# Kernel tuning notes

Hardware: AMD Instinct MI355X
Metric: run time of the kernel (lower is better)

Reference implementation:

```python
import jax, jax.numpy as jnp
import numpy as np


def setup_inputs() -> dict:
    key = jax.random.key(0)
    k1, k2 = jax.random.split(key)
    N, H, W, F = 32, 16, 16, 256
    B, C = 64, 8
    x = jax.random.normal(k1, (N, H, W, F), dtype=jnp.float32)
    # keras 'uniform' initializer: U(-0.05, 0.05)
    T = jax.random.uniform(k2, (F, B, C), dtype=jnp.float32, minval=-0.05, maxval=0.05)
    return {"x": x, "T": T}


def reference(x, T):
    # x: [N,H,W,F], T: [F,B,C]
    M = jnp.einsum('nhwf,fbc->nhwbc', x, T)            # [N,H,W,B,C]
    # all-pairs L1 distance over C between samples i and j
    diff = jnp.abs(M[:, None] - M[None, :])            # [N,N,H,W,B,C]
    norm = jnp.sum(diff, axis=-1)                      # [N,N,H,W,B]
    o_b = jnp.sum(jnp.exp(-norm), axis=1)              # [N,H,W,B]
    return jnp.concatenate([x, o_b], axis=3)           # [N,H,W,F+B]
```

## Files before the change

### kernel.cpp

```cpp
#include <hip/hip_runtime.h>
#include <hip/hip_bf16.h>


namespace {
constexpr int kN = 32;
constexpr int kHW = 256;
constexpr int kF = 256;
constexpr int kOutRow = 320;
constexpr int kMstride = 136;
constexpr int kOstride = 24;
}

using frag_ab = __attribute__((ext_vector_type(8))) short;
using frag_cd = __attribute__((ext_vector_type(4))) float;

__device__ inline unsigned short f2bf(float f) {
  union { __hip_bfloat16 h; unsigned short u; } c;
  c.h = __float2bfloat16(f);
  return c.u;
}

__device__ inline void unpack8(const uint4& m, float* f) {
  f[0] = __uint_as_float(m.x << 16);  f[1] = __uint_as_float(m.x & 0xffff0000u);
  f[2] = __uint_as_float(m.y << 16);  f[3] = __uint_as_float(m.y & 0xffff0000u);
  f[4] = __uint_as_float(m.z << 16);  f[5] = __uint_as_float(m.z & 0xffff0000u);
  f[6] = __uint_as_float(m.w << 16);  f[7] = __uint_as_float(m.w & 0xffff0000u);
}

__global__ __launch_bounds__(256)
void pack_T(const float* __restrict__ T, uint4* __restrict__ Tf) {
  const int g = blockIdx.x * 256 + threadIdx.x;
  const int l = g & 63;
  const int frag = g >> 6;
  const int tt = frag >> 3, kt = frag & 7;
  const int col = tt * 16 + (l & 15);
  const int k0 = kt * 32 + (l >> 4) * 8;
  unsigned p[4];
#pragma unroll
  for (int jj = 0; jj < 4; ++jj) {
    float a = T[(size_t)(k0 + jj * 2) * 512 + col];
    float b = T[(size_t)(k0 + jj * 2 + 1) * 512 + col];
    p[jj] = (unsigned)f2bf(a) | ((unsigned)f2bf(b) << 16);
  }
  Tf[g] = make_uint4(p[0], p[1], p[2], p[3]);
}

__global__ __launch_bounds__(256, 4)
void mbd_main(const float* __restrict__ x, const uint4* __restrict__ Tf,
              float* __restrict__ out) {
  __shared__ uint4 Afrag[2 * 8 * 64];
  __shared__ __align__(16) unsigned short Mlds[kN * kMstride];
  float* obuf = (float*)Afrag;
  const int hw = blockIdx.x & (kHW - 1);
  const int qg = blockIdx.x >> 8;
  const int tid = threadIdx.x;
  const int l = tid & 63, w = tid >> 6;

  uint4 bfr[2][8];
#pragma unroll
  for (int q = 0; q < 2; ++q)
#pragma unroll
    for (int kt = 0; kt < 8; ++kt) {
      const int tT = qg * 8 + w * 2 + q;
      bfr[q][kt] = Tf[(tT * 8 + kt) * 64 + l];
    }

  const float4* x4 = (const float4*)x;
  float4* out4 = (float4*)out;
#pragma unroll
  for (int s = 0; s < 4; ++s) {
    const int task = tid + s * 256;
    const int n = task >> 5;
    const int k8 = task & 31;
    const size_t xb = (size_t)n * (kHW * kF / 4) + (size_t)hw * (kF / 4) + k8 * 2;
    float4 v0 = x4[xb];
    float4 v1 = x4[xb + 1];
    if ((k8 >> 3) == qg) {
      const size_t ob = (size_t)(n * kHW + hw) * (kOutRow / 4) + k8 * 2;
      out4[ob] = v0;
      out4[ob + 1] = v1;
    }
    uint4 p;
    p.x = (unsigned)f2bf(v0.x) | ((unsigned)f2bf(v0.y) << 16);
    p.y = (unsigned)f2bf(v0.z) | ((unsigned)f2bf(v0.w) << 16);
    p.z = (unsigned)f2bf(v1.x) | ((unsigned)f2bf(v1.y) << 16);
    p.w = (unsigned)f2bf(v1.z) | ((unsigned)f2bf(v1.w) << 16);
    const int rt = n >> 4, kt = k8 >> 2, ln = (n & 15) | ((k8 & 3) << 4);
    Afrag[(rt * 8 + kt) * 64 + ln] = p;
  }
  __syncthreads();

  frag_cd acc[2][2] = {};
#pragma unroll
  for (int kt = 0; kt < 8; ++kt) {
    uint4 a0 = Afrag[(0 * 8 + kt) * 64 + l];
    uint4 a1 = Afrag[(1 * 8 + kt) * 64 + l];
    frag_ab af0 = __builtin_bit_cast(frag_ab, a0);
    frag_ab af1 = __builtin_bit_cast(frag_ab, a1);
#pragma unroll
    for (int q = 0; q < 2; ++q) {
      frag_ab bf = __builtin_bit_cast(frag_ab, bfr[q][kt]);
      acc[q][0] = __builtin_amdgcn_mfma_f32_16x16x32_bf16(af0, bf, acc[q][0], 0, 0, 0);
      acc[q][1] = __builtin_amdgcn_mfma_f32_16x16x32_bf16(af1, bf, acc[q][1], 0, 0, 0);
    }
  }

#pragma unroll
  for (int q = 0; q < 2; ++q)
#pragma unroll
    for (int rt = 0; rt < 2; ++rt)
#pragma unroll
      for (int r = 0; r < 4; ++r) {
        const int n = rt * 16 + (l >> 4) * 4 + r;
        const int t = (w * 2 + q) * 16 + (l & 15);
        Mlds[n * kMstride + t] = f2bf(acc[q][rt][r]);
      }
  __syncthreads();

  const int b = tid >> 4;
  const int i0 = (tid & 15) * 2;
  float mi[2][8];
#pragma unroll
  for (int ii = 0; ii < 2; ++ii) {
    uint4 m = *(const uint4*)&Mlds[(i0 + ii) * kMstride + b * 8];
    unpack8(m, mi[ii]);
  }
  float ob0 = 0.f, ob1 = 0.f;
#pragma unroll 4
  for (int j = 0; j < kN; ++j) {
    uint4 m = *(const uint4*)&Mlds[j * kMstride + b * 8];
    float mj[8];
    unpack8(m, mj);
    float n0 = 0.f, n1 = 0.f;
#pragma unroll
    for (int c = 0; c < 8; ++c) {
      n0 += fabsf(mi[0][c] - mj[c]);
      n1 += fabsf(mi[1][c] - mj[c]);
    }
    ob0 += __expf(-n0);
    ob1 += __expf(-n1);
  }
  obuf[i0 * kOstride + b] = ob0;
  obuf[(i0 + 1) * kOstride + b] = ob1;
  __syncthreads();

  if (tid < 128) {
    const int n = tid >> 2;
    const int b4 = tid & 3;
    float4 v = *(const float4*)&obuf[n * kOstride + b4 * 4];
    out4[(size_t)(n * kHW + hw) * (kOutRow / 4) + (kF / 4) + qg * 4 + b4] = v;
  }
}

extern "C" void kernel_launch(void* const* d_in, const int* in_sizes, int n_in,
                              void* d_out, int out_size, void* d_ws, size_t ws_size,
                              hipStream_t stream) {
  const float* x = (const float*)d_in[0];
  const float* T = (const float*)d_in[1];
  float* out = (float*)d_out;
  uint4* Tf = (uint4*)d_ws;
  (void)in_sizes; (void)n_in; (void)out_size; (void)ws_size;
  pack_T<<<dim3(64), dim3(256), 0, stream>>>(T, Tf);
  mbd_main<<<dim3(4 * kHW), dim3(256), 0, stream>>>(x, Tf, out);
}
```

Measured before the change: 77.20 us.

## Load x fragments directly from global per wave, drop LDS A-staging and barrier

The shared-memory staging of bf16 x fragments and its barrier are removed. Each wave now reads its x rows straight from global memory, converts them to bf16 in registers, and swaps the MFMA operand roles so that T is the A operand and x is the B operand. The M write-back indexing is transposed to match. The x passthrough copy now covers only this block's quarter of features. This cuts LDS traffic and one sync, but each of the four waves re-reads the same x data from global/L2, and T fragments are loaded inside the k loop instead of being preloaded.

```diff
diff --git a/kernel.cpp b/kernel.cpp
--- a/kernel.cpp
+++ b/kernel.cpp
@@ -27,6 +27,15 @@
   f[6] = __uint_as_float(m.w << 16);  f[7] = __uint_as_float(m.w & 0xffff0000u);
 }
 
+__device__ inline uint4 pack_bf8(const float4& v0, const float4& v1) {
+  uint4 p;
+  p.x = (unsigned)f2bf(v0.x) | ((unsigned)f2bf(v0.y) << 16);
+  p.y = (unsigned)f2bf(v0.z) | ((unsigned)f2bf(v0.w) << 16);
+  p.z = (unsigned)f2bf(v1.x) | ((unsigned)f2bf(v1.y) << 16);
+  p.w = (unsigned)f2bf(v1.z) | ((unsigned)f2bf(v1.w) << 16);
+  return p;
+}
+
 __global__ __launch_bounds__(256)
 void pack_T(const float* __restrict__ T, uint4* __restrict__ Tf) {
   const int g = blockIdx.x * 256 + threadIdx.x;
@@ -48,72 +57,62 @@
 __global__ __launch_bounds__(256, 4)
 void mbd_main(const float* __restrict__ x, const uint4* __restrict__ Tf,
               float* __restrict__ out) {
-  __shared__ uint4 Afrag[2 * 8 * 64];
   __shared__ __align__(16) unsigned short Mlds[kN * kMstride];
-  float* obuf = (float*)Afrag;
+  __shared__ float obuf[kN * kOstride];
   const int hw = blockIdx.x & (kHW - 1);
   const int qg = blockIdx.x >> 8;
   const int tid = threadIdx.x;
   const int l = tid & 63, w = tid >> 6;
 
-  uint4 bfr[2][8];
-#pragma unroll
-  for (int q = 0; q < 2; ++q)
-#pragma unroll
-    for (int kt = 0; kt < 8; ++kt) {
-      const int tT = qg * 8 + w * 2 + q;
-      bfr[q][kt] = Tf[(tT * 8 + kt) * 64 + l];
-    }
-
   const float4* x4 = (const float4*)x;
   float4* out4 = (float4*)out;
-#pragma unroll
-  for (int s = 0; s < 4; ++s) {
-    const int task = tid + s * 256;
-    const int n = task >> 5;
-    const int k8 = task & 31;
-    const size_t xb = (size_t)n * (kHW * kF / 4) + (size_t)hw * (kF / 4) + k8 * 2;
+
+  {
+    const int n = tid >> 3;
+    const int k8 = tid & 7;
+    const size_t base = (size_t)(n * kHW + hw) * (kF / 4) + qg * 16 + k8 * 2;
+    const size_t xb = (size_t)n * (kHW * kF / 4) + (size_t)hw * (kF / 4) +
+                      qg * 16 + k8 * 2;
     float4 v0 = x4[xb];
     float4 v1 = x4[xb + 1];
-    if ((k8 >> 3) == qg) {
-      const size_t ob = (size_t)(n * kHW + hw) * (kOutRow / 4) + k8 * 2;
-      out4[ob] = v0;
-      out4[ob + 1] = v1;
-    }
-    uint4 p;
-    p.x = (unsigned)f2bf(v0.x) | ((unsigned)f2bf(v0.y) << 16);
-    p.y = (unsigned)f2bf(v0.z) | ((unsigned)f2bf(v0.w) << 16);
-    p.z = (unsigned)f2bf(v1.x) | ((unsigned)f2bf(v1.y) << 16);
-    p.w = (unsigned)f2bf(v1.z) | ((unsigned)f2bf(v1.w) << 16);
-    const int rt = n >> 4, kt = k8 >> 2, ln = (n & 15) | ((k8 & 3) << 4);
-    Afrag[(rt * 8 + kt) * 64 + ln] = p;
+    const size_t ob = (size_t)(n * kHW + hw) * (kOutRow / 4) + qg * 16 + k8 * 2;
+    out4[ob] = v0;
+    out4[ob + 1] = v1;
+    (void)base;
   }
-  __syncthreads();
 
   frag_cd acc[2][2] = {};
+  const size_t xrow0 = ((size_t)((l & 15) + 0) * kHW + hw) * kF + (l >> 4) * 8;
+  const size_t xrow1 = ((size_t)((l & 15) + 16) * kHW + hw) * kF + (l >> 4) * 8;
 #pragma unroll
   for (int kt = 0; kt < 8; ++kt) {
-    uint4 a0 = Afrag[(0 * 8 + kt) * 64 + l];
-    uint4 a1 = Afrag[(1 * 8 + kt) * 64 + l];
-    frag_ab af0 = __builtin_bit_cast(frag_ab, a0);
-    frag_ab af1 = __builtin_bit_cast(frag_ab, a1);
+    float4 b00 = *(const float4*)&x[xrow0 + kt * 32];
+    float4 b01 = *(const float4*)&x[xrow0 + kt * 32 + 4];
+    float4 b10 = *(const float4*)&x[xrow1 + kt * 32];
+    float4 b11 = *(const float4*)&x[xrow1 + kt * 32 + 4];
+    uint4 bn0 = pack_bf8(b00, b01);
+    uint4 bn1 = pack_bf8(b10, b11);
+    frag_ab bf0 = __builtin_bit_cast(frag_ab, bn0);
+    frag_ab bf1 = __builtin_bit_cast(frag_ab, bn1);
 #pragma unroll
     for (int q = 0; q < 2; ++q) {
-      frag_ab bf = __builtin_bit_cast(frag_ab, bfr[q][kt]);
-      acc[q][0] = __builtin_amdgcn_mfma_f32_16x16x32_bf16(af0, bf, acc[q][0], 0, 0, 0);
-      acc[q][1] = __builtin_amdgcn_mfma_f32_16x16x32_bf16(af1, bf, acc[q][1], 0, 0, 0);
+      const int tT = qg * 8 + w * 2 + q;
+      uint4 a = Tf[(tT * 8 + kt) * 64 + l];
+      frag_ab af = __builtin_bit_cast(frag_ab, a);
+      acc[q][0] = __builtin_amdgcn_mfma_f32_16x16x32_bf16(af, bf0, acc[q][0], 0, 0, 0);
+      acc[q][1] = __builtin_amdgcn_mfma_f32_16x16x32_bf16(af, bf1, acc[q][1], 0, 0, 0);
     }
   }
 
 #pragma unroll
   for (int q = 0; q < 2; ++q)
 #pragma unroll
-    for (int rt = 0; rt < 2; ++rt)
+    for (int nt = 0; nt < 2; ++nt)
 #pragma unroll
       for (int r = 0; r < 4; ++r) {
-        const int n = rt * 16 + (l >> 4) * 4 + r;
-        const int t = (w * 2 + q) * 16 + (l & 15);
-        Mlds[n * kMstride + t] = f2bf(acc[q][rt][r]);
+        const int t = (w * 2 + q) * 16 + (l >> 4) * 4 + r;
+        const int n = nt * 16 + (l & 15);
+        Mlds[n * kMstride + t] = f2bf(acc[q][nt][r]);
       }
   __syncthreads();
 
```

After: 85.60 us. 10.9% more time.

## Pre-pack x into bf16 MFMA fragments in a prep kernel and copy passthrough there

Applied to the files above, without the earlier changes.

A combined prep kernel now converts x to bf16 once per hw position, already laid out as MFMA A-fragments in workspace, and also writes the x passthrough columns of the output. The same kernel packs T. The main kernel then loads A-fragments straight from global memory instead of staging fp32 x through LDS with a sync. Before, each of the four blocks per hw reread and converted the full fp32 x slice. The trade is a workspace write and read round trip of the bf16 x (about 8 MB), plus the main kernel reading its fragments from global memory rather than LDS.

```diff
diff --git a/kernel.cpp b/kernel.cpp
--- a/kernel.cpp
+++ b/kernel.cpp
@@ -9,6 +9,7 @@
 constexpr int kOutRow = 320;
 constexpr int kMstride = 136;
 constexpr int kOstride = 24;
+constexpr int kXfFrags = 1024;
 }
 
 using frag_ab = __attribute__((ext_vector_type(8))) short;
@@ -20,6 +21,15 @@
   return c.u;
 }
 
+__device__ inline uint4 pack_bf8(const float4& v0, const float4& v1) {
+  uint4 p;
+  p.x = (unsigned)f2bf(v0.x) | ((unsigned)f2bf(v0.y) << 16);
+  p.y = (unsigned)f2bf(v0.z) | ((unsigned)f2bf(v0.w) << 16);
+  p.z = (unsigned)f2bf(v1.x) | ((unsigned)f2bf(v1.y) << 16);
+  p.w = (unsigned)f2bf(v1.z) | ((unsigned)f2bf(v1.w) << 16);
+  return p;
+}
+
 __device__ inline void unpack8(const uint4& m, float* f) {
   f[0] = __uint_as_float(m.x << 16);  f[1] = __uint_as_float(m.x & 0xffff0000u);
   f[2] = __uint_as_float(m.y << 16);  f[3] = __uint_as_float(m.y & 0xffff0000u);
@@ -28,78 +38,74 @@
 }
 
 __global__ __launch_bounds__(256)
-void pack_T(const float* __restrict__ T, uint4* __restrict__ Tf) {
-  const int g = blockIdx.x * 256 + threadIdx.x;
-  const int l = g & 63;
-  const int frag = g >> 6;
-  const int tt = frag >> 3, kt = frag & 7;
-  const int col = tt * 16 + (l & 15);
-  const int k0 = kt * 32 + (l >> 4) * 8;
-  unsigned p[4];
+void prep(const float* __restrict__ x, const float* __restrict__ T,
+          float* __restrict__ out, uint4* __restrict__ xf,
+          uint4* __restrict__ Tf) {
+  const int tid = threadIdx.x;
+  if (blockIdx.x < 256) {
+    const int hw = blockIdx.x;
+    const int l = tid & 63, w = tid >> 6;
 #pragma unroll
-  for (int jj = 0; jj < 4; ++jj) {
-    float a = T[(size_t)(k0 + jj * 2) * 512 + col];
-    float b = T[(size_t)(k0 + jj * 2 + 1) * 512 + col];
-    p[jj] = (unsigned)f2bf(a) | ((unsigned)f2bf(b) << 16);
+    for (int it = 0; it < 4; ++it) {
+      const int fg = it * 4 + w;
+      const int rt = fg >> 3, kt = fg & 7;
+      const int n = rt * 16 + (l & 15);
+      const int k0 = kt * 32 + (l >> 4) * 8;
+      const float* xp = x + ((size_t)(n * kHW + hw) * kF + k0);
+      float4 v0 = *(const float4*)xp;
+      float4 v1 = *(const float4*)(xp + 4);
+      float* op = out + ((size_t)(n * kHW + hw) * kOutRow + k0);
+      *(float4*)op = v0;
+      *(float4*)(op + 4) = v1;
+      xf[(size_t)hw * kXfFrags + fg * 64 + l] = pack_bf8(v0, v1);
+    }
+  } else {
+    const int g = (blockIdx.x - 256) * 256 + tid;
+    const int l = g & 63;
+    const int frag = g >> 6;
+    const int tt = frag >> 3, kt = frag & 7;
+    const int col = tt * 16 + (l & 15);
+    const int k0 = kt * 32 + (l >> 4) * 8;
+    unsigned p[4];
+#pragma unroll
+    for (int jj = 0; jj < 4; ++jj) {
+      float a = T[(size_t)(k0 + jj * 2) * 512 + col];
+      float b = T[(size_t)(k0 + jj * 2 + 1) * 512 + col];
+      p[jj] = (unsigned)f2bf(a) | ((unsigned)f2bf(b) << 16);
+    }
+    Tf[g] = make_uint4(p[0], p[1], p[2], p[3]);
   }
-  Tf[g] = make_uint4(p[0], p[1], p[2], p[3]);
 }
 
 __global__ __launch_bounds__(256, 4)
-void mbd_main(const float* __restrict__ x, const uint4* __restrict__ Tf,
+void mbd_main(const uint4* __restrict__ xf, const uint4* __restrict__ Tf,
               float* __restrict__ out) {
-  __shared__ uint4 Afrag[2 * 8 * 64];
   __shared__ __align__(16) unsigned short Mlds[kN * kMstride];
-  float* obuf = (float*)Afrag;
+  __shared__ float obuf[kN * kOstride];
   const int hw = blockIdx.x & (kHW - 1);
   const int qg = blockIdx.x >> 8;
   const int tid = threadIdx.x;
   const int l = tid & 63, w = tid >> 6;
 
-  uint4 bfr[2][8];
+  uint4 Bf[2][8];
 #pragma unroll
-  for (int q = 0; q < 2; ++q)
+  for (int q = 0; q < 2; ++q) {
+    const int tT = qg * 8 + w * 2 + q;
 #pragma unroll
-    for (int kt = 0; kt < 8; ++kt) {
-      const int tT = qg * 8 + w * 2 + q;
-      bfr[q][kt] = Tf[(tT * 8 + kt) * 64 + l];
-    }
+    for (int kt = 0; kt < 8; ++kt) Bf[q][kt] = Tf[(tT * 8 + kt) * 64 + l];
+  }
 
-  const float4* x4 = (const float4*)x;
-  float4* out4 = (float4*)out;
-#pragma unroll
-  for (int s = 0; s < 4; ++s) {
-    const int task = tid + s * 256;
-    const int n = task >> 5;
-    const int k8 = task & 31;
-    const size_t xb = (size_t)n * (kHW * kF / 4) + (size_t)hw * (kF / 4) + k8 * 2;
-    float4 v0 = x4[xb];
-    float4 v1 = x4[xb + 1];
-    if ((k8 >> 3) == qg) {
-      const size_t ob = (size_t)(n * kHW + hw) * (kOutRow / 4) + k8 * 2;
-      out4[ob] = v0;
-      out4[ob + 1] = v1;
-    }
-    uint4 p;
-    p.x = (unsigned)f2bf(v0.x) | ((unsigned)f2bf(v0.y) << 16);
-    p.y = (unsigned)f2bf(v0.z) | ((unsigned)f2bf(v0.w) << 16);
-    p.z = (unsigned)f2bf(v1.x) | ((unsigned)f2bf(v1.y) << 16);
-    p.w = (unsigned)f2bf(v1.z) | ((unsigned)f2bf(v1.w) << 16);
-    const int rt = n >> 4, kt = k8 >> 2, ln = (n & 15) | ((k8 & 3) << 4);
-    Afrag[(rt * 8 + kt) * 64 + ln] = p;
-  }
-  __syncthreads();
-
+  const uint4* xfp = xf + (size_t)hw * kXfFrags + l;
   frag_cd acc[2][2] = {};
 #pragma unroll
   for (int kt = 0; kt < 8; ++kt) {
-    uint4 a0 = Afrag[(0 * 8 + kt) * 64 + l];
-    uint4 a1 = Afrag[(1 * 8 + kt) * 64 + l];
+    uint4 a0 = xfp[(0 * 8 + kt) * 64];
+    uint4 a1 = xfp[(1 * 8 + kt) * 64];
     frag_ab af0 = __builtin_bit_cast(frag_ab, a0);
     frag_ab af1 = __builtin_bit_cast(frag_ab, a1);
 #pragma unroll
     for (int q = 0; q < 2; ++q) {
-      frag_ab bf = __builtin_bit_cast(frag_ab, bfr[q][kt]);
+      frag_ab bf = __builtin_bit_cast(frag_ab, Bf[q][kt]);
       acc[q][0] = __builtin_amdgcn_mfma_f32_16x16x32_bf16(af0, bf, acc[q][0], 0, 0, 0);
       acc[q][1] = __builtin_amdgcn_mfma_f32_16x16x32_bf16(af1, bf, acc[q][1], 0, 0, 0);
     }
@@ -148,7 +154,7 @@
     const int n = tid >> 2;
     const int b4 = tid & 3;
     float4 v = *(const float4*)&obuf[n * kOstride + b4 * 4];
-    out4[(size_t)(n * kHW + hw) * (kOutRow / 4) + (kF / 4) + qg * 4 + b4] = v;
+    *(float4*)&out[(size_t)(n * kHW + hw) * kOutRow + kF + qg * 16 + b4 * 4] = v;
   }
 }
 
@@ -158,8 +164,9 @@
   const float* x = (const float*)d_in[0];
   const float* T = (const float*)d_in[1];
   float* out = (float*)d_out;
-  uint4* Tf = (uint4*)d_ws;
+  uint4* xf = (uint4*)d_ws;
+  uint4* Tf = (uint4*)d_ws + (size_t)kHW * kXfFrags;
   (void)in_sizes; (void)n_in; (void)out_size; (void)ws_size;
-  pack_T<<<dim3(64), dim3(256), 0, stream>>>(T, Tf);
-  mbd_main<<<dim3(4 * kHW), dim3(256), 0, stream>>>(x, Tf, out);
+  prep<<<dim3(320), dim3(256), 0, stream>>>(x, T, out, xf, Tf);
+  mbd_main<<<dim3(4 * kHW), dim3(256), 0, stream>>>(xf, Tf, out);
 }
```

New measurement: 78.73 us. Within noise of the previous version (+2.0%).
